# Kernel optimization log

Hardware: AMD Instinct MI355X
Metric: run time of the kernel (lower is better)

The kernel has to match this reference:

```python
import jax, jax.numpy as jnp
import numpy as np

B, I, H = 32768, 1024, 1024

def _xavier(key, shape):
    fan_out, fan_in = shape
    limit = float(np.sqrt(6.0 / (fan_in + fan_out)))
    return jax.random.uniform(key, shape, jnp.float32, -limit, limit)

def setup_inputs() -> dict:
    key = jax.random.key(0)
    ks = jax.random.split(key, 8)
    return {
        "x": jax.random.normal(ks[0], (B, I), jnp.float32),
        "h": jax.random.normal(ks[1], (B, H), jnp.float32),
        "weight_ir": _xavier(ks[2], (H, I)),
        "weight_hr": _xavier(ks[3], (H, H)),
        "weight_iz": _xavier(ks[4], (H, I)),
        "weight_hz": _xavier(ks[5], (H, H)),
        "weight_in": _xavier(ks[6], (H, I)),
        "weight_hn": _xavier(ks[7], (H, H)),
        "bias_ir": jnp.zeros((H,), jnp.float32),
        "bias_hr": jnp.zeros((H,), jnp.float32),
        "bias_iz": jnp.zeros((H,), jnp.float32),
        "bias_hz": jnp.zeros((H,), jnp.float32),
        "bias_in": jnp.zeros((H,), jnp.float32),
        "bias_hn": jnp.zeros((H,), jnp.float32),
    }

def reference(x, h, weight_ir, weight_hr, weight_iz, weight_hz, weight_in, weight_hn,
              bias_ir, bias_hr, bias_iz, bias_hz, bias_in, bias_hn):
    # Fuse the 3 input-side and 3 hidden-side GEMMs into two concatenated GEMMs
    # (same math as 6 separate F.linear calls).
    Wi = jnp.concatenate([weight_ir, weight_iz, weight_in], axis=0)  # [3H, I]
    Wh = jnp.concatenate([weight_hr, weight_hz, weight_hn], axis=0)  # [3H, H]
    bi = jnp.concatenate([bias_ir, bias_iz, bias_in])
    bh = jnp.concatenate([bias_hr, bias_hz, bias_hn])
    gi = x @ Wi.T + bi   # [B, 3H]
    gh = h @ Wh.T + bh   # [B, 3H]
    Hd = weight_hr.shape[0]
    ir, iz, inn = gi[:, :Hd], gi[:, Hd:2*Hd], gi[:, 2*Hd:]
    hr, hz, hn = gh[:, :Hd], gh[:, Hd:2*Hd], gh[:, 2*Hd:]
    r = jax.nn.sigmoid(ir + hr)
    z = jax.nn.sigmoid(iz + hz)
    n = jnp.tanh(inn + r * hn)
    return (1.0 - z) * n + z * h
```

## Files before the change

kernel.cpp:

```cpp
#include <hip/hip_runtime.h>
#include <hip/hip_bf16.h>


#define B_ROWS 32768
#define KD     1024
#define HD     1024

#define BM 128
#define BN 64
#define BK 32

typedef __bf16 bf16_t;
typedef __bf16 bf16x8 __attribute__((ext_vector_type(8)));
typedef __bf16 bf16x4 __attribute__((ext_vector_type(4)));
typedef float  f32x4  __attribute__((ext_vector_type(4)));

#define XT_BYTES  67108864ull
#define WT_OFF   134217728ull
#define WS_NEEDED 146800640ull

#define X_SLOTS 4194304
#define W_BASE_SLOT 8388608
#define TOTAL_SLOTS 9175040

__device__ __forceinline__ float sigm_f(float v) { return 1.0f / (1.0f + __expf(-v)); }
__device__ __forceinline__ float tanh_f(float v) { return 2.0f / (1.0f + __expf(-2.0f * v)) - 1.0f; }

__device__ __forceinline__ bf16x4 cvt4(f32x4 v) {
    bf16x4 r;
    r[0] = (bf16_t)v[0]; r[1] = (bf16_t)v[1];
    r[2] = (bf16_t)v[2]; r[3] = (bf16_t)v[3];
    return r;
}

__device__ __forceinline__ void glds16(const void* g, void* l) {
    __builtin_amdgcn_global_load_lds(
        (const __attribute__((address_space(1))) void*)g,
        (__attribute__((address_space(3))) void*)l, 16, 0, 0);
}

struct WPtrs { const float* p[6]; };

__global__ void __launch_bounds__(256)
cvt_kernel(const float* __restrict__ x, const float* __restrict__ h,
           WPtrs wp, bf16_t* __restrict__ ws)
{
    int sid = blockIdx.x * 256 + threadIdx.x;
    if (sid >= TOTAL_SLOTS) return;

    const float* src;
    if (sid < W_BASE_SLOT) {
        const float* base = (sid < X_SLOTS) ? x : h;
        int s2   = sid & (X_SLOTS - 1);
        int tile = s2 >> 9;
        int c    = s2 & 511;
        int row  = c >> 2, s = c & 3;
        int mt   = tile >> 5, kt = tile & 31;
        int ks   = s ^ ((row >> 1) & 3);
        src = base + (size_t)(mt * 128 + row) * KD + kt * 32 + ks * 8;
    } else {
        int s2   = sid - W_BASE_SLOT;
        int tile = s2 / 1536;
        int c    = s2 % 1536;
        int g    = c >> 8;
        int cc   = c & 255;
        int row  = cc >> 2, s = cc & 3;
        int nt   = tile >> 5, kt = tile & 31;
        int ks   = s ^ ((row >> 1) & 3);
        src = wp.p[g] + (size_t)(nt * 64 + row) * KD + kt * 32 + ks * 8;
    }
    f32x4 a = *(const f32x4*)src;
    f32x4 b = *(const f32x4*)(src + 4);
    bf16x8 o;
    o[0]=(bf16_t)a[0]; o[1]=(bf16_t)a[1]; o[2]=(bf16_t)a[2]; o[3]=(bf16_t)a[3];
    o[4]=(bf16_t)b[0]; o[5]=(bf16_t)b[1]; o[6]=(bf16_t)b[2]; o[7]=(bf16_t)b[3];
    *(bf16x8*)(ws + (size_t)sid * 8) = o;
}

__global__ void __launch_bounds__(256, 2)
gru_mfma_kernel(const bf16_t* __restrict__ xt, const bf16_t* __restrict__ ht,
                const bf16_t* __restrict__ wt,
                const float* __restrict__ h,
                const float* __restrict__ b_ir, const float* __restrict__ b_hr,
                const float* __restrict__ b_iz, const float* __restrict__ b_hz,
                const float* __restrict__ b_in, const float* __restrict__ b_hn,
                float* __restrict__ out)
{
    __shared__ __align__(16) char smem[40960];

    const int tid  = threadIdx.x;
    const int lane = tid & 63;
    const int wid  = tid >> 6;
    const int wr   = wid >> 1;
    const int wc   = wid & 1;

    const int nblk = HD / BN;
    const int bidN = blockIdx.x % nblk;
    const int bidM = blockIdx.x / nblk;
    const int rowBase = bidM * BM;
    const int colBase = bidN * BN;

    const char* xcb = (const char*)xt + (size_t)bidM * 32 * 8192;
    const char* hcb = (const char*)ht + (size_t)bidM * 32 * 8192;
    const char* wcb = (const char*)wt + (size_t)bidN * 32 * 24576;

    const f32x4 vzero = {0.f, 0.f, 0.f, 0.f};
    f32x4 accR[4][2], accZ[4][2], accIN[4][2], accHN[4][2];
    #pragma unroll
    for (int m = 0; m < 4; ++m)
        #pragma unroll
        for (int n = 0; n < 2; ++n) {
            accR[m][n] = vzero; accZ[m][n] = vzero;
            accIN[m][n] = vzero; accHN[m][n] = vzero;
        }

    const int fr  = lane & 15;
    const int sl  = lane >> 4;
    const int f   = (fr >> 1) & 3;
    const int col = ((sl ^ f) << 4);
    int aoff[4], boff[2];
    #pragma unroll
    for (int m = 0; m < 4; ++m) aoff[m] = (wr * 64 + m * 16 + fr) * 64 + col;
    #pragma unroll
    for (int n = 0; n < 2; ++n) boff[n] = (wc * 32 + n * 16 + fr) * 64 + col;

    for (int kt = 0; kt < 32; ++kt) {
        const char* xc = xcb + (size_t)kt * 8192;
        const char* hc = hcb + (size_t)kt * 8192;
        const char* wc2 = wcb + (size_t)kt * 24576;

        #pragma unroll
        for (int i = 0; i < 2; ++i) {
            int off = wid * 2048 + i * 1024;
            glds16(xc + off + lane * 16, smem + off);
            glds16(hc + off + lane * 16, smem + 8192 + off);
        }
        #pragma unroll
        for (int j = 0; j < 6; ++j) {
            int off = wid * 6144 + j * 1024;
            glds16(wc2 + off + lane * 16, smem + 16384 + off);
        }
        __syncthreads();

        bf16x8 xa[4], ha[4];
        #pragma unroll
        for (int m = 0; m < 4; ++m) {
            xa[m] = *(const bf16x8*)(smem + aoff[m]);
            ha[m] = *(const bf16x8*)(smem + 8192 + aoff[m]);
        }
        bf16x8 wb[6][2];
        #pragma unroll
        for (int g = 0; g < 6; ++g)
            #pragma unroll
            for (int n = 0; n < 2; ++n)
                wb[g][n] = *(const bf16x8*)(smem + 16384 + g * 4096 + boff[n]);

        #pragma unroll
        for (int m = 0; m < 4; ++m) {
            #pragma unroll
            for (int n = 0; n < 2; ++n) {
                accR[m][n]  = __builtin_amdgcn_mfma_f32_16x16x32_bf16(xa[m], wb[0][n], accR[m][n], 0, 0, 0);
                accR[m][n]  = __builtin_amdgcn_mfma_f32_16x16x32_bf16(ha[m], wb[1][n], accR[m][n], 0, 0, 0);
                accZ[m][n]  = __builtin_amdgcn_mfma_f32_16x16x32_bf16(xa[m], wb[2][n], accZ[m][n], 0, 0, 0);
                accZ[m][n]  = __builtin_amdgcn_mfma_f32_16x16x32_bf16(ha[m], wb[3][n], accZ[m][n], 0, 0, 0);
                accIN[m][n] = __builtin_amdgcn_mfma_f32_16x16x32_bf16(xa[m], wb[4][n], accIN[m][n], 0, 0, 0);
                accHN[m][n] = __builtin_amdgcn_mfma_f32_16x16x32_bf16(ha[m], wb[5][n], accHN[m][n], 0, 0, 0);
            }
        }
        __syncthreads();
    }

    const int rq = (lane >> 4) * 4;
    float br[2], bz[2], bi[2], bh[2];
    #pragma unroll
    for (int n = 0; n < 2; ++n) {
        int c = colBase + wc * 32 + n * 16 + fr;
        br[n] = b_ir[c] + b_hr[c];
        bz[n] = b_iz[c] + b_hz[c];
        bi[n] = b_in[c];
        bh[n] = b_hn[c];
    }
    #pragma unroll
    for (int m = 0; m < 4; ++m) {
        #pragma unroll
        for (int n = 0; n < 2; ++n) {
            int gc = colBase + wc * 32 + n * 16 + fr;
            #pragma unroll
            for (int j = 0; j < 4; ++j) {
                int gr = rowBase + wr * 64 + m * 16 + rq + j;
                float rv = sigm_f(accR[m][n][j] + br[n]);
                float zv = sigm_f(accZ[m][n][j] + bz[n]);
                float nv = tanh_f(accIN[m][n][j] + bi[n] + rv * (accHN[m][n][j] + bh[n]));
                float hv = h[(size_t)gr * HD + gc];
                out[(size_t)gr * HD + gc] = (1.0f - zv) * nv + zv * hv;
            }
        }
    }
}

#define PK 40
__global__ void __launch_bounds__(256, 2)
gru_fused_kernel(const float* __restrict__ x,  const float* __restrict__ h,
                 const float* __restrict__ w_ir, const float* __restrict__ w_hr,
                 const float* __restrict__ w_iz, const float* __restrict__ w_hz,
                 const float* __restrict__ w_in, const float* __restrict__ w_hn,
                 const float* __restrict__ b_ir, const float* __restrict__ b_hr,
                 const float* __restrict__ b_iz, const float* __restrict__ b_hz,
                 const float* __restrict__ b_in, const float* __restrict__ b_hn,
                 float* __restrict__ out)
{
    __shared__ __align__(16) bf16_t xs[BM][PK];
    __shared__ __align__(16) bf16_t hs[BM][PK];
    __shared__ __align__(16) bf16_t ws[6][BN][PK];

    const int tid  = threadIdx.x;
    const int lane = tid & 63;
    const int wid  = tid >> 6;
    const int wr   = wid >> 1;
    const int wc   = wid & 1;

    const int nblk = HD / BN;
    const int bidN = blockIdx.x % nblk;
    const int bidM = blockIdx.x / nblk;
    const int rowBase = bidM * BM;
    const int colBase = bidN * BN;

    const float* wptr[6] = { w_ir, w_hr, w_iz, w_hz, w_in, w_hn };

    int sr[4], sc[4];
    #pragma unroll
    for (int i = 0; i < 4; ++i) {
        int idx = tid + i * 256;
        sr[i] = idx >> 3;
        sc[i] = (idx & 7) * 4;
    }
    int xoff[4];
    #pragma unroll
    for (int i = 0; i < 4; ++i) xoff[i] = (rowBase + sr[i]) * KD + sc[i];
    int woff[2];
    #pragma unroll
    for (int i = 0; i < 2; ++i) woff[i] = (colBase + sr[i]) * KD + sc[i];

    const f32x4 vzero = {0.f, 0.f, 0.f, 0.f};
    f32x4 accR[4][2], accZ[4][2], accIN[4][2], accHN[4][2];
    #pragma unroll
    for (int m = 0; m < 4; ++m)
        #pragma unroll
        for (int n = 0; n < 2; ++n) {
            accR[m][n] = vzero; accZ[m][n] = vzero;
            accIN[m][n] = vzero; accHN[m][n] = vzero;
        }

    const int fr = lane & 15;
    const int ko = (lane >> 4) * 8;

    for (int k0 = 0; k0 < KD; k0 += BK) {
        __syncthreads();
        #pragma unroll
        for (int i = 0; i < 4; ++i) {
            f32x4 vx = *(const f32x4*)&x[xoff[i] + k0];
            f32x4 vh = *(const f32x4*)&h[xoff[i] + k0];
            *(bf16x4*)&xs[sr[i]][sc[i]] = cvt4(vx);
            *(bf16x4*)&hs[sr[i]][sc[i]] = cvt4(vh);
        }
        #pragma unroll
        for (int g = 0; g < 6; ++g) {
            #pragma unroll
            for (int i = 0; i < 2; ++i) {
                f32x4 vw = *(const f32x4*)&wptr[g][woff[i] + k0];
                *(bf16x4*)&ws[g][sr[i]][sc[i]] = cvt4(vw);
            }
        }
        __syncthreads();

        bf16x8 xa[4], ha[4];
        #pragma unroll
        for (int m = 0; m < 4; ++m) {
            xa[m] = *(const bf16x8*)&xs[wr * 64 + m * 16 + fr][ko];
            ha[m] = *(const bf16x8*)&hs[wr * 64 + m * 16 + fr][ko];
        }
        bf16x8 wb[6][2];
        #pragma unroll
        for (int g = 0; g < 6; ++g)
            #pragma unroll
            for (int n = 0; n < 2; ++n)
                wb[g][n] = *(const bf16x8*)&ws[g][wc * 32 + n * 16 + fr][ko];

        #pragma unroll
        for (int m = 0; m < 4; ++m) {
            #pragma unroll
            for (int n = 0; n < 2; ++n) {
                accR[m][n]  = __builtin_amdgcn_mfma_f32_16x16x32_bf16(xa[m], wb[0][n], accR[m][n], 0, 0, 0);
                accR[m][n]  = __builtin_amdgcn_mfma_f32_16x16x32_bf16(ha[m], wb[1][n], accR[m][n], 0, 0, 0);
                accZ[m][n]  = __builtin_amdgcn_mfma_f32_16x16x32_bf16(xa[m], wb[2][n], accZ[m][n], 0, 0, 0);
                accZ[m][n]  = __builtin_amdgcn_mfma_f32_16x16x32_bf16(ha[m], wb[3][n], accZ[m][n], 0, 0, 0);
                accIN[m][n] = __builtin_amdgcn_mfma_f32_16x16x32_bf16(xa[m], wb[4][n], accIN[m][n], 0, 0, 0);
                accHN[m][n] = __builtin_amdgcn_mfma_f32_16x16x32_bf16(ha[m], wb[5][n], accHN[m][n], 0, 0, 0);
            }
        }
    }

    const int rq = (lane >> 4) * 4;
    float br[2], bz[2], bi[2], bh[2];
    #pragma unroll
    for (int n = 0; n < 2; ++n) {
        int c = colBase + wc * 32 + n * 16 + fr;
        br[n] = b_ir[c] + b_hr[c];
        bz[n] = b_iz[c] + b_hz[c];
        bi[n] = b_in[c];
        bh[n] = b_hn[c];
    }
    #pragma unroll
    for (int m = 0; m < 4; ++m) {
        #pragma unroll
        for (int n = 0; n < 2; ++n) {
            int gc = colBase + wc * 32 + n * 16 + fr;
            #pragma unroll
            for (int j = 0; j < 4; ++j) {
                int gr = rowBase + wr * 64 + m * 16 + rq + j;
                float rv = sigm_f(accR[m][n][j] + br[n]);
                float zv = sigm_f(accZ[m][n][j] + bz[n]);
                float nv = tanh_f(accIN[m][n][j] + bi[n] + rv * (accHN[m][n][j] + bh[n]));
                float hv = h[gr * HD + gc];
                out[gr * HD + gc] = (1.0f - zv) * nv + zv * hv;
            }
        }
    }
}

extern "C" void kernel_launch(void* const* d_in, const int* in_sizes, int n_in,
                              void* d_out, int out_size, void* d_ws, size_t ws_size,
                              hipStream_t stream) {
    const float* x    = (const float*)d_in[0];
    const float* h    = (const float*)d_in[1];
    const float* w_ir = (const float*)d_in[2];
    const float* w_hr = (const float*)d_in[3];
    const float* w_iz = (const float*)d_in[4];
    const float* w_hz = (const float*)d_in[5];
    const float* w_in = (const float*)d_in[6];
    const float* w_hn = (const float*)d_in[7];
    const float* b_ir = (const float*)d_in[8];
    const float* b_hr = (const float*)d_in[9];
    const float* b_iz = (const float*)d_in[10];
    const float* b_hz = (const float*)d_in[11];
    const float* b_in = (const float*)d_in[12];
    const float* b_hn = (const float*)d_in[13];
    float* out = (float*)d_out;

    if (ws_size >= WS_NEEDED) {
        bf16_t* ws = (bf16_t*)d_ws;
        WPtrs wp;
        wp.p[0] = w_ir; wp.p[1] = w_hr; wp.p[2] = w_iz;
        wp.p[3] = w_hz; wp.p[4] = w_in; wp.p[5] = w_hn;
        cvt_kernel<<<(TOTAL_SLOTS + 255) / 256, 256, 0, stream>>>(x, h, wp, ws);

        const bf16_t* xt = ws;
        const bf16_t* ht = ws + XT_BYTES / 2;
        const bf16_t* wt = ws + WT_OFF / 2;
        dim3 grid((B_ROWS / BM) * (HD / BN));
        gru_mfma_kernel<<<grid, 256, 0, stream>>>(
            xt, ht, wt, h, b_ir, b_hr, b_iz, b_hz, b_in, b_hn, out);
    } else {
        dim3 grid((B_ROWS / BM) * (HD / BN));
        gru_fused_kernel<<<grid, 256, 0, stream>>>(
            x, h, w_ir, w_hr, w_iz, w_hz, w_in, w_hn,
            b_ir, b_hr, b_iz, b_hz, b_in, b_hn, out);
    }
}
```

Before: 520.0 us.

## Double-buffer LDS tiles to overlap global loads with MFMA compute

Splits the K-loop into a load stage and a compute stage over two LDS buffers. The next tile's direct-to-LDS loads are issued before the current tile is computed, and a partial vmcnt wait keeps only the latest stage in flight. The aim is to hide global memory latency behind MFMA work. It doubles LDS usage per block, which may constrain occupancy.

```diff
diff --git a/kernel.cpp b/kernel.cpp
--- a/kernel.cpp
+++ b/kernel.cpp
@@ -86,7 +86,7 @@
                 const float* __restrict__ b_in, const float* __restrict__ b_hn,
                 float* __restrict__ out)
 {
-    __shared__ __align__(16) char smem[40960];
+    __shared__ __align__(16) char smem[2][40960];
 
     const int tid  = threadIdx.x;
     const int lane = tid & 63;
@@ -124,36 +124,37 @@
     #pragma unroll
     for (int n = 0; n < 2; ++n) boff[n] = (wc * 32 + n * 16 + fr) * 64 + col;
 
-    for (int kt = 0; kt < 32; ++kt) {
-        const char* xc = xcb + (size_t)kt * 8192;
-        const char* hc = hcb + (size_t)kt * 8192;
+    auto STAGE = [&](int buf, int kt) {
+        const char* xc  = xcb + (size_t)kt * 8192;
+        const char* hc  = hcb + (size_t)kt * 8192;
         const char* wc2 = wcb + (size_t)kt * 24576;
-
+        char* s = smem[buf];
         #pragma unroll
         for (int i = 0; i < 2; ++i) {
             int off = wid * 2048 + i * 1024;
-            glds16(xc + off + lane * 16, smem + off);
-            glds16(hc + off + lane * 16, smem + 8192 + off);
+            glds16(xc + off + lane * 16, s + off);
+            glds16(hc + off + lane * 16, s + 8192 + off);
         }
         #pragma unroll
         for (int j = 0; j < 6; ++j) {
             int off = wid * 6144 + j * 1024;
-            glds16(wc2 + off + lane * 16, smem + 16384 + off);
-        }
-        __syncthreads();
-
+            glds16(wc2 + off + lane * 16, s + 16384 + off);
+        }
+    };
+
+    auto COMPUTE = [&](const char* s) {
         bf16x8 xa[4], ha[4];
         #pragma unroll
         for (int m = 0; m < 4; ++m) {
-            xa[m] = *(const bf16x8*)(smem + aoff[m]);
-            ha[m] = *(const bf16x8*)(smem + 8192 + aoff[m]);
+            xa[m] = *(const bf16x8*)(s + aoff[m]);
+            ha[m] = *(const bf16x8*)(s + 8192 + aoff[m]);
         }
         bf16x8 wb[6][2];
         #pragma unroll
         for (int g = 0; g < 6; ++g)
             #pragma unroll
             for (int n = 0; n < 2; ++n)
-                wb[g][n] = *(const bf16x8*)(smem + 16384 + g * 4096 + boff[n]);
+                wb[g][n] = *(const bf16x8*)(s + 16384 + g * 4096 + boff[n]);
 
         #pragma unroll
         for (int m = 0; m < 4; ++m) {
@@ -167,8 +168,23 @@
                 accHN[m][n] = __builtin_amdgcn_mfma_f32_16x16x32_bf16(ha[m], wb[5][n], accHN[m][n], 0, 0, 0);
             }
         }
-        __syncthreads();
-    }
+    };
+
+    STAGE(0, 0);
+
+    for (int kt = 0; kt < 31; ++kt) {
+        STAGE((kt + 1) & 1, kt + 1);
+        asm volatile("s_waitcnt vmcnt(10)" ::: "memory");
+        __builtin_amdgcn_s_barrier();
+        __builtin_amdgcn_sched_barrier(0);
+        COMPUTE(smem[kt & 1]);
+        __builtin_amdgcn_sched_barrier(0);
+        __builtin_amdgcn_s_barrier();
+    }
+    asm volatile("s_waitcnt vmcnt(0)" ::: "memory");
+    __builtin_amdgcn_s_barrier();
+    __builtin_amdgcn_sched_barrier(0);
+    COMPUTE(smem[1]);
 
     const int rq = (lane >> 4) * 4;
     float br[2], bz[2], bi[2], bh[2];
```

Measured after the change: 473.2 us (median of 2 runs). 1.1x faster.
